# Kernel optimization log

Hardware: AMD Instinct MI355X
Metric: run time of the kernel (lower is better)

## Reference

```python
import jax, jax.numpy as jnp
import numpy as np

B = 4096        # batch
STOCH = 1024    # 32x32 stoch
ACT = 32        # action dim
DETER = 4096
TOKENS = 16
D = DETER // TOKENS   # token_dim = 256
S = 256               # state_size
L = 4                 # layers
EPS = 1e-4


def rmsnorm(x, w):
    # torch.nn.RMSNorm with eps=1e-4, elementwise affine weight, no bias
    return x * jax.lax.rsqrt(jnp.mean(x * x, axis=-1, keepdims=True) + EPS) * w


def setup_inputs() -> dict:
    key = jax.random.key(0)
    ks = jax.random.split(key, 12)

    def w(k, shape, scale=0.02):
        return jax.random.normal(k, shape, dtype=jnp.float32) * scale

    return {
        "stoch": jax.random.normal(ks[0], (B, STOCH), dtype=jnp.float32),
        "deter": jax.random.normal(ks[1], (B, DETER), dtype=jnp.float32),
        "action": jax.random.normal(ks[2], (B, ACT), dtype=jnp.float32),
        # input_proj: Linear(stoch+act -> D), RMSNorm(D), SiLU
        "W0": w(ks[3], (D, STOCH + ACT)),
        "b0": jnp.zeros((D,), jnp.float32),
        "g0": jnp.ones((D,), jnp.float32),
        # per-layer S4Block params, stacked over L layers
        "norm_w": jnp.ones((L, D), jnp.float32),
        "W_in": w(ks[4], (L, S, D)),
        "b_in": jnp.zeros((L, S), jnp.float32),
        "W_out": w(ks[5], (L, D, S)),
        "b_out": jnp.zeros((L, D), jnp.float32),
        "W_skip": w(ks[6], (L, D, D)),
        "b_skip": jnp.zeros((L, D), jnp.float32),
        "log_decay": jnp.zeros((L, S), jnp.float32),
        "out_norm_w": jnp.ones((D,), jnp.float32),
    }


def reference(stoch, deter, action, W0, b0, g0, norm_w, W_in, b_in,
              W_out, b_out, W_skip, b_skip, log_decay, out_norm_w):
    bsz = action.shape[0]
    # action / clip(|action|, min=1).detach()
    a = action / jax.lax.stop_gradient(jnp.maximum(jnp.abs(action), 1.0))
    h = jnp.concatenate([stoch.reshape(bsz, -1), a], axis=-1) @ W0.T + b0
    new_tok = jax.nn.silu(rmsnorm(h, g0))                       # [B, D]
    tokens = deter.reshape(bsz, TOKENS, D)
    tokens = jnp.concatenate([tokens[:, 1:], new_tok[:, None]], axis=1)  # [B, T, D]

    def s4_block(tokens, params):
        nw, Wi, bi, Wo, bo, Ws, bsk, ld = params
        x = rmsnorm(tokens, nw)                                 # [B, T, D]
        u = jnp.einsum('btd,sd->tbs', x, Wi) + bi               # [T, B, S]
        decay = jax.nn.sigmoid(ld)                              # [S]

        def step(state, u_t):
            state = decay * state + u_t
            return state, state

        init = jnp.zeros((bsz, Wi.shape[0]), dtype=x.dtype)
        _, states = jax.lax.scan(step, init, u)                 # [T, B, S]
        out = (jnp.einsum('tbs,ds->btd', states, Wo) + bo
               + jnp.einsum('btd,ed->bte', x, Ws) + bsk)
        return tokens + out, None

    tokens, _ = jax.lax.scan(
        s4_block, tokens,
        (norm_w, W_in, b_in, W_out, b_out, W_skip, b_skip, log_decay))
    tokens = rmsnorm(tokens, out_norm_w)
    return tokens.reshape(bsz, -1)
```

## Files before the change

### kernel.cpp

```cpp
#include <hip/hip_runtime.h>
#include <hip/hip_bf16.h>
#include <stdint.h>

#define NB   4096
#define NTOK 16
#define ND   256
#define NS   256
#define NL   4
#define KIN  1056
#define RMS_EPS 1e-4f

typedef float f32x4 __attribute__((ext_vector_type(4)));
typedef short s16x8 __attribute__((ext_vector_type(8)));

__device__ __forceinline__ unsigned short f2bf(float f) {
    unsigned u = __float_as_uint(f);
    u += 0x7fff + ((u >> 16) & 1);
    return (unsigned short)(u >> 16);
}


__global__ __launch_bounds__(256) void k_cast(const float* __restrict__ src,
                                              unsigned short* __restrict__ dst, int n) {
    for (int i = blockIdx.x * blockDim.x + threadIdx.x; i < n; i += gridDim.x * blockDim.x)
        dst[i] = f2bf(src[i]);
}

__global__ __launch_bounds__(256) void k_build_a0(const float* __restrict__ stoch,
                                                  const float* __restrict__ act,
                                                  unsigned short* __restrict__ a0) {
    int total = NB * KIN;
    for (int i = blockIdx.x * blockDim.x + threadIdx.x; i < total; i += gridDim.x * blockDim.x) {
        int b = i / KIN, k = i - b * KIN;
        float v;
        if (k < 1024) v = stoch[b * 1024 + k];
        else { float a = act[b * 32 + (k - 1024)]; v = a / fmaxf(fabsf(a), 1.0f); }
        a0[i] = f2bf(v);
    }
}

#define KP 40
__device__ __forceinline__ void gemm_chunked(const unsigned short* __restrict__ A,
                                             const unsigned short* __restrict__ W,
                                             int K, int m0, int n0,
                                             unsigned short* lds, f32x4 acc[4][2]) {
    const int tid = threadIdx.x;
    const int lane = tid & 63;
    const int wvid = tid >> 6;
    const int wm = wvid & 1, wn = wvid >> 1;
    const int srow = tid >> 2, skk = (tid & 3) * 8;
    const int mbase = m0 + wm * 64 + (lane & 15);
    const int koff = (lane >> 4) * 8;
    const int brow = wn * 32 + (lane & 15);
    for (int kc = 0; kc < K; kc += 32) {
        __syncthreads();
        *reinterpret_cast<s16x8*>(&lds[srow * KP + skk]) =
            *reinterpret_cast<const s16x8*>(&W[(size_t)(n0 + srow) * K + kc + skk]);
        __syncthreads();
        s16x8 a[4];
#pragma unroll
        for (int mf = 0; mf < 4; mf++)
            a[mf] = *reinterpret_cast<const s16x8*>(&A[(size_t)(mbase + mf * 16) * K + kc + koff]);
#pragma unroll
        for (int nf = 0; nf < 2; nf++) {
            s16x8 bfr = *reinterpret_cast<const s16x8*>(&lds[(brow + nf * 16) * KP + koff]);
#pragma unroll
            for (int mf = 0; mf < 4; mf++)
                acc[mf][nf] = __builtin_amdgcn_mfma_f32_16x16x32_bf16(a[mf], bfr, acc[mf][nf], 0, 0, 0);
        }
    }
}

__global__ __launch_bounds__(256) void k_gemm_h(const unsigned short* __restrict__ A0,
                                                const unsigned short* __restrict__ W0bf,
                                                const float* __restrict__ b0,
                                                float* __restrict__ h) {
    __shared__ unsigned short lds[64 * KP];
    f32x4 acc[4][2];
#pragma unroll
    for (int i = 0; i < 4; i++)
#pragma unroll
        for (int j = 0; j < 2; j++) acc[i][j] = (f32x4){0.f, 0.f, 0.f, 0.f};
    int m0 = blockIdx.x * 128, n0 = blockIdx.y * 64;
    gemm_chunked(A0, W0bf, KIN, m0, n0, lds, acc);
    int lane = threadIdx.x & 63, wvid = threadIdx.x >> 6;
    int wm = wvid & 1, wn = wvid >> 1;
    int rbase = m0 + wm * 64 + (lane >> 4) * 4;
    int cbase = n0 + wn * 32 + (lane & 15);
#pragma unroll
    for (int mf = 0; mf < 4; mf++)
#pragma unroll
        for (int nf = 0; nf < 2; nf++) {
            int col = cbase + nf * 16;
            float bb = b0[col];
#pragma unroll
            for (int r = 0; r < 4; r++)
                h[(size_t)(rbase + mf * 16 + r) * ND + col] = acc[mf][nf][r] + bb;
        }
}

__global__ __launch_bounds__(256) void k_h_norm(const float* __restrict__ X,
                                                const float* __restrict__ wg,
                                                float* __restrict__ ntok) {
    int row = blockIdx.x * 4 + (threadIdx.x >> 6);
    int lane = threadIdx.x & 63;
    float4 v = reinterpret_cast<const float4*>(X)[(size_t)row * 64 + lane];
    float ss = v.x * v.x + v.y * v.y + v.z * v.z + v.w * v.w;
#pragma unroll
    for (int off = 32; off > 0; off >>= 1) ss += __shfl_xor(ss, off);
    float scale = rsqrtf(ss * (1.0f / 256.0f) + RMS_EPS);
    float4 wv = reinterpret_cast<const float4*>(wg)[lane];
    float o0 = v.x * scale * wv.x, o1 = v.y * scale * wv.y;
    float o2 = v.z * scale * wv.z, o3 = v.w * scale * wv.w;
    float4 q;
    q.x = o0 / (1.f + expf(-o0));
    q.y = o1 / (1.f + expf(-o1));
    q.z = o2 / (1.f + expf(-o2));
    q.w = o3 / (1.f + expf(-o3));
    reinterpret_cast<float4*>(ntok)[(size_t)row * 64 + lane] = q;
}


#define LSTR 264

__device__ __forceinline__ void gemm_pass(const unsigned short* lds_a,
                                          const unsigned short* __restrict__ B,
                                          int w, int q, int g, f32x4 acc[4][4]) {
    const unsigned short* bp = B + (size_t)(w * 64 + q) * 256 + g * 8;
    const unsigned short* ap = lds_a + q * LSTR + g * 8;
#pragma unroll 2
    for (int kc = 0; kc < 256; kc += 32) {
        s16x8 bw[4];
#pragma unroll
        for (int nf = 0; nf < 4; nf++)
            bw[nf] = *reinterpret_cast<const s16x8*>(bp + nf * (16 * 256) + kc);
#pragma unroll
        for (int mf = 0; mf < 4; mf++) {
            s16x8 a = *reinterpret_cast<const s16x8*>(ap + mf * (16 * LSTR) + kc);
#pragma unroll
            for (int nf = 0; nf < 4; nf++)
                acc[mf][nf] = __builtin_amdgcn_mfma_f32_16x16x32_bf16(a, bw[nf], acc[mf][nf], 0, 0, 0);
        }
    }
}

__global__ __launch_bounds__(256, 2) void k_mega(
    const float* __restrict__ deter, const float* __restrict__ ntok,
    const unsigned short* __restrict__ Win, const unsigned short* __restrict__ Wout,
    const unsigned short* __restrict__ Wskip,
    const float* __restrict__ norm_w, const float* __restrict__ b_in,
    const float* __restrict__ b_out, const float* __restrict__ b_skip,
    const float* __restrict__ log_dec, const float* __restrict__ out_nw,
    float* __restrict__ out)
{
    __shared__ __align__(16) unsigned short xs[64 * LSTR];
    __shared__ __align__(16) unsigned short st[64 * LSTR];
    __shared__ __align__(16) float red[4 * 64 + 64];

    const int tid = threadIdx.x;
    const int lane = tid & 63;
    const int w = tid >> 6;
    const int g = lane >> 4;
    const int q = lane & 15;
    const int e = lane & 1;
    const int b0 = blockIdx.x * 4;
    const int lm16 = (lane - 16) & 63, lm32 = (lane - 32) & 63, lm48 = (lane - 48) & 63;

    f32x4 tok[4][4];
#pragma unroll
    for (int mf = 0; mf < 4; mf++) {
        const float* dbase = deter + (size_t)(b0 + mf) * 4096;
        const float* nbase = ntok + (size_t)(b0 + mf) * 256;
#pragma unroll
        for (int nf = 0; nf < 4; nf++) {
            int col = w * 64 + nf * 16 + q;
#pragma unroll
            for (int r = 0; r < 4; r++) {
                int t = g * 4 + r;
                tok[mf][nf][r] = (t < 15) ? dbase[(t + 1) * 256 + col] : nbase[col];
            }
        }
    }

    float scale[4][4];

    auto rms_scale = [&]() {
#pragma unroll
        for (int mf = 0; mf < 4; mf++) {
            f32x4 p = (f32x4){0.f, 0.f, 0.f, 0.f};
#pragma unroll
            for (int nf = 0; nf < 4; nf++)
#pragma unroll
                for (int r = 0; r < 4; r++) p[r] += tok[mf][nf][r] * tok[mf][nf][r];
#pragma unroll
            for (int mask = 1; mask < 16; mask <<= 1) {
#pragma unroll
                for (int r = 0; r < 4; r++) p[r] += __shfl_xor(p[r], mask);
            }
            if (q == 0) *reinterpret_cast<f32x4*>(&red[w * 64 + mf * 16 + g * 4]) = p;
        }
        __syncthreads();
        if (tid < 64) {
            float s = red[tid] + red[64 + tid] + red[128 + tid] + red[192 + tid];
            red[256 + tid] = rsqrtf(s * (1.0f / 256.0f) + RMS_EPS);
        }
        __syncthreads();
#pragma unroll
        for (int mf = 0; mf < 4; mf++) {
            f32x4 sc = *reinterpret_cast<const f32x4*>(&red[256 + mf * 16 + g * 4]);
#pragma unroll
            for (int r = 0; r < 4; r++) scale[mf][r] = sc[r];
        }
    };

    auto scat = [&](unsigned short* dst, float vE, float vO, int mf, int r, int nf2) {
        float oE = __shfl_xor(vE, 1);
        float oO = __shfl_xor(vO, 1);
        float lo = e ? oO : vE;
        float hi = e ? vO : oE;
        unsigned pk = (unsigned)f2bf(lo) | ((unsigned)f2bf(hi) << 16);
        int m = mf * 16 + g * 4 + r;
        int colb = w * 64 + (nf2 * 2 + e) * 16 + (q & ~1);
        *reinterpret_cast<unsigned*>(&dst[m * LSTR + colb]) = pk;
    };

    for (int l = 0; l < NL; l++) {
        const unsigned short* Wi = Win + (size_t)l * 65536;
        const unsigned short* Wo = Wout + (size_t)l * 65536;
        const unsigned short* Ws = Wskip + (size_t)l * 65536;
        float nw[4], bi[4], dec[4], bo[4];
#pragma unroll
        for (int nf = 0; nf < 4; nf++) {
            int col = w * 64 + nf * 16 + q;
            nw[nf] = norm_w[l * 256 + col];
            bi[nf] = b_in[l * 256 + col];
            dec[nf] = 1.f / (1.f + expf(-log_dec[l * 256 + col]));
            bo[nf] = b_out[l * 256 + col] + b_skip[l * 256 + col];
        }

        rms_scale();
#pragma unroll
        for (int mf = 0; mf < 4; mf++)
#pragma unroll
            for (int r = 0; r < 4; r++)
#pragma unroll
                for (int nf2 = 0; nf2 < 2; nf2++) {
                    float vE = tok[mf][nf2 * 2][r] * scale[mf][r] * nw[nf2 * 2];
                    float vO = tok[mf][nf2 * 2 + 1][r] * scale[mf][r] * nw[nf2 * 2 + 1];
                    scat(xs, vE, vO, mf, r, nf2);
                }
        __syncthreads();

        f32x4 acc[4][4];
#pragma unroll
        for (int i = 0; i < 4; i++)
#pragma unroll
            for (int j = 0; j < 4; j++) acc[i][j] = (f32x4){0.f, 0.f, 0.f, 0.f};
        gemm_pass(xs, Wi, w, q, g, acc);

#pragma unroll
        for (int mf = 0; mf < 4; mf++)
#pragma unroll
            for (int nf = 0; nf < 4; nf++) {
                float d1 = dec[nf], dd2 = d1 * d1, dd3 = dd2 * d1, dd4 = dd2 * dd2, dd8 = dd4 * dd4;
                f32x4& u = acc[mf][nf];
                float s0 = u[0] + bi[nf];
                float s1 = u[1] + bi[nf] + d1 * s0;
                float s2 = u[2] + bi[nf] + d1 * s1;
                float s3 = u[3] + bi[nf] + d1 * s2;
                float Q = s3;
                float q1 = __shfl(Q, lm16); q1 = (g >= 1) ? q1 : 0.f;
                float q2 = __shfl(Q, lm32); q2 = (g >= 2) ? q2 : 0.f;
                float q3 = __shfl(Q, lm48); q3 = (g >= 3) ? q3 : 0.f;
                float carry = q1 + dd4 * q2 + dd8 * q3;
                u[0] = s0 + d1 * carry;
                u[1] = s1 + dd2 * carry;
                u[2] = s2 + dd3 * carry;
                u[3] = s3 + dd4 * carry;
            }

#pragma unroll
        for (int mf = 0; mf < 4; mf++)
#pragma unroll
            for (int r = 0; r < 4; r++)
#pragma unroll
                for (int nf2 = 0; nf2 < 2; nf2++)
                    scat(st, acc[mf][nf2 * 2][r], acc[mf][nf2 * 2 + 1][r], mf, r, nf2);
        __syncthreads();

#pragma unroll
        for (int i = 0; i < 4; i++)
#pragma unroll
            for (int j = 0; j < 4; j++) acc[i][j] = (f32x4){0.f, 0.f, 0.f, 0.f};
        gemm_pass(st, Wo, w, q, g, acc);
        gemm_pass(xs, Ws, w, q, g, acc);
#pragma unroll
        for (int mf = 0; mf < 4; mf++)
#pragma unroll
            for (int nf = 0; nf < 4; nf++)
#pragma unroll
                for (int r = 0; r < 4; r++)
                    tok[mf][nf][r] += acc[mf][nf][r] + bo[nf];
    }

    rms_scale();
    float onw[4];
#pragma unroll
    for (int nf = 0; nf < 4; nf++) onw[nf] = out_nw[w * 64 + nf * 16 + q];
#pragma unroll
    for (int mf = 0; mf < 4; mf++) {
        float* obase = out + (size_t)(b0 + mf) * 4096;
#pragma unroll
        for (int r = 0; r < 4; r++)
#pragma unroll
            for (int nf2 = 0; nf2 < 2; nf2++) {
                float vE = tok[mf][nf2 * 2][r] * scale[mf][r] * onw[nf2 * 2];
                float vO = tok[mf][nf2 * 2 + 1][r] * scale[mf][r] * onw[nf2 * 2 + 1];
                float oE = __shfl_xor(vE, 1);
                float oO = __shfl_xor(vO, 1);
                float lo = e ? oO : vE;
                float hi = e ? vO : oE;
                int colb = w * 64 + (nf2 * 2 + e) * 16 + (q & ~1);
                float2 val = make_float2(lo, hi);
                *reinterpret_cast<float2*>(&obase[(g * 4 + r) * 256 + colb]) = val;
            }
    }
}


extern "C" void kernel_launch(void* const* d_in, const int* in_sizes, int n_in,
                              void* d_out, int out_size, void* d_ws, size_t ws_size,
                              hipStream_t stream) {
    const float* stoch   = (const float*)d_in[0];
    const float* deter   = (const float*)d_in[1];
    const float* action  = (const float*)d_in[2];
    const float* W0      = (const float*)d_in[3];
    const float* b0      = (const float*)d_in[4];
    const float* g0      = (const float*)d_in[5];
    const float* norm_w  = (const float*)d_in[6];
    const float* W_in    = (const float*)d_in[7];
    const float* b_in    = (const float*)d_in[8];
    const float* W_out   = (const float*)d_in[9];
    const float* b_out   = (const float*)d_in[10];
    const float* W_skip  = (const float*)d_in[11];
    const float* b_skip  = (const float*)d_in[12];
    const float* log_dec = (const float*)d_in[13];
    const float* onw     = (const float*)d_in[14];
    float* out = (float*)d_out;

    unsigned short* A0bf    = (unsigned short*)d_ws;
    unsigned short* W0bf    = A0bf + (size_t)NB * KIN;
    unsigned short* Winbf   = W0bf + (size_t)256 * KIN;
    unsigned short* Woutbf  = Winbf + (size_t)NL * 65536;
    unsigned short* Wskipbf = Woutbf + (size_t)NL * 65536;
    float* hbuf = (float*)(Wskipbf + (size_t)NL * 65536);
    float* ntok = hbuf + (size_t)NB * 256;

    k_cast<<<512, 256, 0, stream>>>(W0, W0bf, 256 * KIN);
    k_cast<<<512, 256, 0, stream>>>(W_in, Winbf, NL * 65536);
    k_cast<<<512, 256, 0, stream>>>(W_out, Woutbf, NL * 65536);
    k_cast<<<512, 256, 0, stream>>>(W_skip, Wskipbf, NL * 65536);
    k_build_a0<<<2048, 256, 0, stream>>>(stoch, action, A0bf);

    k_gemm_h<<<dim3(NB / 128, 4), 256, 0, stream>>>(A0bf, W0bf, b0, hbuf);
    k_h_norm<<<NB / 4, 256, 0, stream>>>(hbuf, g0, ntok);

    k_mega<<<1024, 256, 0, stream>>>(deter, ntok, Winbf, Woutbf, Wskipbf,
                                     norm_w, b_in, b_out, b_skip, log_dec, onw, out);
}
```

Before: 392.5 us.

## Split mega kernel across 8 waves, share one LDS buffer, fuse weight casts

```diff
diff --git a/kernel.cpp b/kernel.cpp
--- a/kernel.cpp
+++ b/kernel.cpp
@@ -20,10 +20,23 @@
 }
 
 
-__global__ __launch_bounds__(256) void k_cast(const float* __restrict__ src,
-                                              unsigned short* __restrict__ dst, int n) {
-    for (int i = blockIdx.x * blockDim.x + threadIdx.x; i < n; i += gridDim.x * blockDim.x)
-        dst[i] = f2bf(src[i]);
+__global__ __launch_bounds__(256) void k_cast4(const float* __restrict__ W0,
+                                               const float* __restrict__ Wi,
+                                               const float* __restrict__ Wo,
+                                               const float* __restrict__ Ws,
+                                               unsigned short* __restrict__ dst) {
+    const int n0 = 256 * KIN;
+    const int nw = NL * 65536;
+    const int total = n0 + 3 * nw;
+    for (int i = blockIdx.x * blockDim.x + threadIdx.x; i < total; i += gridDim.x * blockDim.x) {
+        float v;
+        if (i < n0) v = W0[i];
+        else {
+            int j = i - n0;
+            v = (j < nw) ? Wi[j] : (j < 2 * nw ? Wo[j - nw] : Ws[j - 2 * nw]);
+        }
+        dst[i] = f2bf(v);
+    }
 }
 
 __global__ __launch_bounds__(256) void k_build_a0(const float* __restrict__ stoch,
@@ -112,39 +125,18 @@
     float4 wv = reinterpret_cast<const float4*>(wg)[lane];
     float o0 = v.x * scale * wv.x, o1 = v.y * scale * wv.y;
     float o2 = v.z * scale * wv.z, o3 = v.w * scale * wv.w;
-    float4 q;
-    q.x = o0 / (1.f + expf(-o0));
-    q.y = o1 / (1.f + expf(-o1));
-    q.z = o2 / (1.f + expf(-o2));
-    q.w = o3 / (1.f + expf(-o3));
-    reinterpret_cast<float4*>(ntok)[(size_t)row * 64 + lane] = q;
+    float4 qq;
+    qq.x = o0 / (1.f + expf(-o0));
+    qq.y = o1 / (1.f + expf(-o1));
+    qq.z = o2 / (1.f + expf(-o2));
+    qq.w = o3 / (1.f + expf(-o3));
+    reinterpret_cast<float4*>(ntok)[(size_t)row * 64 + lane] = qq;
 }
 
 
 #define LSTR 264
 
-__device__ __forceinline__ void gemm_pass(const unsigned short* lds_a,
-                                          const unsigned short* __restrict__ B,
-                                          int w, int q, int g, f32x4 acc[4][4]) {
-    const unsigned short* bp = B + (size_t)(w * 64 + q) * 256 + g * 8;
-    const unsigned short* ap = lds_a + q * LSTR + g * 8;
-#pragma unroll 2
-    for (int kc = 0; kc < 256; kc += 32) {
-        s16x8 bw[4];
-#pragma unroll
-        for (int nf = 0; nf < 4; nf++)
-            bw[nf] = *reinterpret_cast<const s16x8*>(bp + nf * (16 * 256) + kc);
-#pragma unroll
-        for (int mf = 0; mf < 4; mf++) {
-            s16x8 a = *reinterpret_cast<const s16x8*>(ap + mf * (16 * LSTR) + kc);
-#pragma unroll
-            for (int nf = 0; nf < 4; nf++)
-                acc[mf][nf] = __builtin_amdgcn_mfma_f32_16x16x32_bf16(a, bw[nf], acc[mf][nf], 0, 0, 0);
-        }
-    }
-}
-
-__global__ __launch_bounds__(256, 2) void k_mega(
+__global__ __launch_bounds__(512, 4) void k_mega(
     const float* __restrict__ deter, const float* __restrict__ ntok,
     const unsigned short* __restrict__ Win, const unsigned short* __restrict__ Wout,
     const unsigned short* __restrict__ Wskip,
@@ -154,26 +146,24 @@
     float* __restrict__ out)
 {
     __shared__ __align__(16) unsigned short xs[64 * LSTR];
-    __shared__ __align__(16) unsigned short st[64 * LSTR];
-    __shared__ __align__(16) float red[4 * 64 + 64];
+    __shared__ __align__(16) float red[8 * 64 + 64];
 
     const int tid = threadIdx.x;
     const int lane = tid & 63;
     const int w = tid >> 6;
     const int g = lane >> 4;
     const int q = lane & 15;
-    const int e = lane & 1;
     const int b0 = blockIdx.x * 4;
     const int lm16 = (lane - 16) & 63, lm32 = (lane - 32) & 63, lm48 = (lane - 48) & 63;
 
-    f32x4 tok[4][4];
+    f32x4 tok[4][2];
 #pragma unroll
     for (int mf = 0; mf < 4; mf++) {
         const float* dbase = deter + (size_t)(b0 + mf) * 4096;
         const float* nbase = ntok + (size_t)(b0 + mf) * 256;
 #pragma unroll
-        for (int nf = 0; nf < 4; nf++) {
-            int col = w * 64 + nf * 16 + q;
+        for (int nf = 0; nf < 2; nf++) {
+            int col = w * 32 + nf * 16 + q;
 #pragma unroll
             for (int r = 0; r < 4; r++) {
                 int t = g * 4 + r;
@@ -187,11 +177,10 @@
     auto rms_scale = [&]() {
 #pragma unroll
         for (int mf = 0; mf < 4; mf++) {
-            f32x4 p = (f32x4){0.f, 0.f, 0.f, 0.f};
-#pragma unroll
-            for (int nf = 0; nf < 4; nf++)
-#pragma unroll
-                for (int r = 0; r < 4; r++) p[r] += tok[mf][nf][r] * tok[mf][nf][r];
+            f32x4 p;
+#pragma unroll
+            for (int r = 0; r < 4; r++)
+                p[r] = tok[mf][0][r] * tok[mf][0][r] + tok[mf][1][r] * tok[mf][1][r];
 #pragma unroll
             for (int mask = 1; mask < 16; mask <<= 1) {
 #pragma unroll
@@ -201,37 +190,44 @@
         }
         __syncthreads();
         if (tid < 64) {
-            float s = red[tid] + red[64 + tid] + red[128 + tid] + red[192 + tid];
-            red[256 + tid] = rsqrtf(s * (1.0f / 256.0f) + RMS_EPS);
+            float s = 0.f;
+#pragma unroll
+            for (int j = 0; j < 8; j++) s += red[j * 64 + tid];
+            red[512 + tid] = rsqrtf(s * (1.0f / 256.0f) + RMS_EPS);
         }
         __syncthreads();
 #pragma unroll
         for (int mf = 0; mf < 4; mf++) {
-            f32x4 sc = *reinterpret_cast<const f32x4*>(&red[256 + mf * 16 + g * 4]);
+            f32x4 sc = *reinterpret_cast<const f32x4*>(&red[512 + mf * 16 + g * 4]);
 #pragma unroll
             for (int r = 0; r < 4; r++) scale[mf][r] = sc[r];
         }
     };
 
-    auto scat = [&](unsigned short* dst, float vE, float vO, int mf, int r, int nf2) {
-        float oE = __shfl_xor(vE, 1);
-        float oO = __shfl_xor(vO, 1);
-        float lo = e ? oO : vE;
-        float hi = e ? vO : oE;
-        unsigned pk = (unsigned)f2bf(lo) | ((unsigned)f2bf(hi) << 16);
-        int m = mf * 16 + g * 4 + r;
-        int colb = w * 64 + (nf2 * 2 + e) * 16 + (q & ~1);
-        *reinterpret_cast<unsigned*>(&dst[m * LSTR + colb]) = pk;
+    auto gemm = [&](const unsigned short* __restrict__ Bmat, f32x4 acc[4][2]) {
+        const unsigned short* bp = Bmat + (size_t)(w * 32 + q) * 256 + g * 8;
+        const unsigned short* ap = xs + q * LSTR + g * 8;
+#pragma unroll 2
+        for (int kc = 0; kc < 256; kc += 32) {
+            s16x8 bw0 = *reinterpret_cast<const s16x8*>(bp + kc);
+            s16x8 bw1 = *reinterpret_cast<const s16x8*>(bp + 16 * 256 + kc);
+#pragma unroll
+            for (int mf = 0; mf < 4; mf++) {
+                s16x8 a = *reinterpret_cast<const s16x8*>(ap + mf * (16 * LSTR) + kc);
+                acc[mf][0] = __builtin_amdgcn_mfma_f32_16x16x32_bf16(a, bw0, acc[mf][0], 0, 0, 0);
+                acc[mf][1] = __builtin_amdgcn_mfma_f32_16x16x32_bf16(a, bw1, acc[mf][1], 0, 0, 0);
+            }
+        }
     };
 
     for (int l = 0; l < NL; l++) {
         const unsigned short* Wi = Win + (size_t)l * 65536;
         const unsigned short* Wo = Wout + (size_t)l * 65536;
         const unsigned short* Ws = Wskip + (size_t)l * 65536;
-        float nw[4], bi[4], dec[4], bo[4];
-#pragma unroll
-        for (int nf = 0; nf < 4; nf++) {
-            int col = w * 64 + nf * 16 + q;
+        float nw[2], bi[2], dec[2], bo[2];
+#pragma unroll
+        for (int nf = 0; nf < 2; nf++) {
+            int col = w * 32 + nf * 16 + q;
             nw[nf] = norm_w[l * 256 + col];
             bi[nf] = b_in[l * 256 + col];
             dec[nf] = 1.f / (1.f + expf(-log_dec[l * 256 + col]));
@@ -242,26 +238,27 @@
 #pragma unroll
         for (int mf = 0; mf < 4; mf++)
 #pragma unroll
-            for (int r = 0; r < 4; r++)
-#pragma unroll
-                for (int nf2 = 0; nf2 < 2; nf2++) {
-                    float vE = tok[mf][nf2 * 2][r] * scale[mf][r] * nw[nf2 * 2];
-                    float vO = tok[mf][nf2 * 2 + 1][r] * scale[mf][r] * nw[nf2 * 2 + 1];
-                    scat(xs, vE, vO, mf, r, nf2);
-                }
-        __syncthreads();
-
-        f32x4 acc[4][4];
+            for (int r = 0; r < 4; r++) {
+                int m = mf * 16 + g * 4 + r;
+#pragma unroll
+                for (int nf = 0; nf < 2; nf++)
+                    xs[m * LSTR + w * 32 + nf * 16 + q] = f2bf(tok[mf][nf][r] * scale[mf][r] * nw[nf]);
+            }
+        __syncthreads();
+
+        gemm(Ws, tok);
+
+        f32x4 acc[4][2];
 #pragma unroll
         for (int i = 0; i < 4; i++)
 #pragma unroll
-            for (int j = 0; j < 4; j++) acc[i][j] = (f32x4){0.f, 0.f, 0.f, 0.f};
-        gemm_pass(xs, Wi, w, q, g, acc);
-
-#pragma unroll
-        for (int mf = 0; mf < 4; mf++)
-#pragma unroll
-            for (int nf = 0; nf < 4; nf++) {
+            for (int j = 0; j < 2; j++) acc[i][j] = (f32x4){0.f, 0.f, 0.f, 0.f};
+        gemm(Wi, acc);
+
+#pragma unroll
+        for (int mf = 0; mf < 4; mf++)
+#pragma unroll
+            for (int nf = 0; nf < 2; nf++) {
                 float d1 = dec[nf], dd2 = d1 * d1, dd3 = dd2 * d1, dd4 = dd2 * dd2, dd8 = dd4 * dd4;
                 f32x4& u = acc[mf][nf];
                 float s0 = u[0] + bi[nf];
@@ -279,51 +276,41 @@
                 u[3] = s3 + dd4 * carry;
             }
 
-#pragma unroll
-        for (int mf = 0; mf < 4; mf++)
-#pragma unroll
-            for (int r = 0; r < 4; r++)
-#pragma unroll
-                for (int nf2 = 0; nf2 < 2; nf2++)
-                    scat(st, acc[mf][nf2 * 2][r], acc[mf][nf2 * 2 + 1][r], mf, r, nf2);
-        __syncthreads();
-
-#pragma unroll
-        for (int i = 0; i < 4; i++)
-#pragma unroll
-            for (int j = 0; j < 4; j++) acc[i][j] = (f32x4){0.f, 0.f, 0.f, 0.f};
-        gemm_pass(st, Wo, w, q, g, acc);
-        gemm_pass(xs, Ws, w, q, g, acc);
-#pragma unroll
-        for (int mf = 0; mf < 4; mf++)
-#pragma unroll
-            for (int nf = 0; nf < 4; nf++)
+        __syncthreads();
+#pragma unroll
+        for (int mf = 0; mf < 4; mf++)
+#pragma unroll
+            for (int r = 0; r < 4; r++) {
+                int m = mf * 16 + g * 4 + r;
+#pragma unroll
+                for (int nf = 0; nf < 2; nf++)
+                    xs[m * LSTR + w * 32 + nf * 16 + q] = f2bf(acc[mf][nf][r]);
+            }
+        __syncthreads();
+
+        gemm(Wo, tok);
+#pragma unroll
+        for (int mf = 0; mf < 4; mf++)
+#pragma unroll
+            for (int nf = 0; nf < 2; nf++)
 #pragma unroll
                 for (int r = 0; r < 4; r++)
-                    tok[mf][nf][r] += acc[mf][nf][r] + bo[nf];
+                    tok[mf][nf][r] += bo[nf];
     }
 
     rms_scale();
-    float onw[4];
-#pragma unroll
-    for (int nf = 0; nf < 4; nf++) onw[nf] = out_nw[w * 64 + nf * 16 + q];
+    float onw[2];
+#pragma unroll
+    for (int nf = 0; nf < 2; nf++) onw[nf] = out_nw[w * 32 + nf * 16 + q];
 #pragma unroll
     for (int mf = 0; mf < 4; mf++) {
         float* obase = out + (size_t)(b0 + mf) * 4096;
 #pragma unroll
         for (int r = 0; r < 4; r++)
 #pragma unroll
-            for (int nf2 = 0; nf2 < 2; nf2++) {
-                float vE = tok[mf][nf2 * 2][r] * scale[mf][r] * onw[nf2 * 2];
-                float vO = tok[mf][nf2 * 2 + 1][r] * scale[mf][r] * onw[nf2 * 2 + 1];
-                float oE = __shfl_xor(vE, 1);
-                float oO = __shfl_xor(vO, 1);
-                float lo = e ? oO : vE;
-                float hi = e ? vO : oE;
-                int colb = w * 64 + (nf2 * 2 + e) * 16 + (q & ~1);
-                float2 val = make_float2(lo, hi);
-                *reinterpret_cast<float2*>(&obase[(g * 4 + r) * 256 + colb]) = val;
-            }
+            for (int nf = 0; nf < 2; nf++)
+                obase[(g * 4 + r) * 256 + w * 32 + nf * 16 + q] =
+                    tok[mf][nf][r] * scale[mf][r] * onw[nf];
     }
 }
 
@@ -356,15 +343,12 @@
     float* hbuf = (float*)(Wskipbf + (size_t)NL * 65536);
     float* ntok = hbuf + (size_t)NB * 256;
 
-    k_cast<<<512, 256, 0, stream>>>(W0, W0bf, 256 * KIN);
-    k_cast<<<512, 256, 0, stream>>>(W_in, Winbf, NL * 65536);
-    k_cast<<<512, 256, 0, stream>>>(W_out, Woutbf, NL * 65536);
-    k_cast<<<512, 256, 0, stream>>>(W_skip, Wskipbf, NL * 65536);
+    k_cast4<<<1024, 256, 0, stream>>>(W0, W_in, W_out, W_skip, W0bf);
     k_build_a0<<<2048, 256, 0, stream>>>(stoch, action, A0bf);
 
     k_gemm_h<<<dim3(NB / 128, 4), 256, 0, stream>>>(A0bf, W0bf, b0, hbuf);
     k_h_norm<<<NB / 4, 256, 0, stream>>>(hbuf, g0, ntok);
 
-    k_mega<<<1024, 256, 0, stream>>>(deter, ntok, Winbf, Woutbf, Wskipbf,
+    k_mega<<<1024, 512, 0, stream>>>(deter, ntok, Winbf, Woutbf, Wskipbf,
                                      norm_w, b_in, b_out, b_skip, log_dec, onw, out);
 }
```

After: 378.1 us. 1.04x faster.
